# Kernel tuning notes

Hardware: AMD Instinct MI355X
Metric: run time of the kernel (lower is better)

Reference implementation:

```python
import jax, jax.numpy as jnp
import numpy as np

NUM_LAYERS = 3
DROPOUT = 0.0  # set to 0 for deterministic reference (torch F.dropout uses its own RNG)


def _spmm(rows, cols, vals, X, n_rows):
    # sparse [n_rows, n_cols] @ X[n_cols, D] via gather + segment_sum
    return jax.ops.segment_sum(vals[:, None] * X[cols], rows, num_segments=n_rows)


def setup_inputs() -> dict:
    key = jax.random.key(0)
    k1, k2, k3, k4, k5 = jax.random.split(key, 5)
    P, U, NNZ, D = 100000, 50000, 2000000, 128
    pois_embs = jax.random.normal(k1, (P, D), dtype=jnp.float32)
    up_rows = jax.random.randint(k2, (NNZ,), 0, U, dtype=jnp.int32)
    up_cols = jax.random.randint(k3, (NNZ,), 0, P, dtype=jnp.int32)
    up_vals = jax.random.uniform(k4, (NNZ,), dtype=jnp.float32)
    pu_vals = jax.random.uniform(k5, (NNZ,), dtype=jnp.float32)
    return {
        "pois_embs": pois_embs,
        "pad_all_train_sessions": jnp.zeros((1,), dtype=jnp.int64),
        "up_rows": up_rows,
        "up_cols": up_cols,
        "up_vals": up_vals,
        "pu_vals": pu_vals,
        "n_users": U,
        "n_pois": P,
    }


def reference(pois_embs, pad_all_train_sessions, up_rows, up_cols, up_vals, pu_vals, n_users, n_pois):
    # HG_up: [U, P] with entries (up_rows, up_cols, up_vals)
    # HG_pu: [P, U] = transpose structure with values pu_vals
    x = pois_embs
    acc = pois_embs  # running sum over layer outputs (incl. layer 0)
    for _ in range(NUM_LAYERS):
        msg = _spmm(up_rows, up_cols, up_vals, x, n_users)          # [U, D]
        prop = _spmm(up_cols, up_rows, pu_vals, msg, n_pois)        # [P, D]
        x = prop + x                                                 # residual
        # dropout with p=DROPOUT=0.0 -> identity
        acc = acc + x
    return acc / jnp.asarray(NUM_LAYERS + 1, dtype=pois_embs.dtype)
```

## Files before the change

kernel.cpp:

```cpp
#include <hip/hip_runtime.h>

#define DD 128
#define NUM_LAYERS 3
#define SCAN_B 1024
#define BKT_SHIFT 7
#define BKT_ROWS 128
#define LDS_BKT 1280
#define EPB 4096
#define SHARDS 4
#define CAP_SUB 1792

typedef unsigned int uint;

__device__ __forceinline__ uint f2bf(float f) {
    uint u = __float_as_uint(f);
    return (u + 0x7fffu + ((u >> 16) & 1u)) >> 16;
}
__device__ __forceinline__ uint pk2(float a, float b) {
    return f2bf(a) | (f2bf(b) << 16);
}
__device__ __forceinline__ void fma8(float acc[8], uint4 q, float v) {
    acc[0] += v * __uint_as_float(q.x << 16);
    acc[1] += v * __uint_as_float(q.x & 0xffff0000u);
    acc[2] += v * __uint_as_float(q.y << 16);
    acc[3] += v * __uint_as_float(q.y & 0xffff0000u);
    acc[4] += v * __uint_as_float(q.z << 16);
    acc[5] += v * __uint_as_float(q.z & 0xffff0000u);
    acc[6] += v * __uint_as_float(q.w << 16);
    acc[7] += v * __uint_as_float(q.w & 0xffff0000u);
}


__global__ void pass1_kernel(const int* __restrict__ up_rows,
                             const int* __restrict__ up_cols,
                             const float* __restrict__ up_vals,
                             const float* __restrict__ pu_vals,
                             int* __restrict__ bkcur,
                             int2* __restrict__ stage,
                             int nnz, int U, int nbkt) {
    __shared__ int lcnt[LDS_BKT];
    const int tid = threadIdx.x;
    const int e0 = blockIdx.x * EPB;
    const int shard = blockIdx.x & (SHARDS - 1);
    for (int i = tid; i < nbkt; i += 256) lcnt[i] = 0;
    __syncthreads();
    #pragma unroll
    for (int i = 0; i < EPB / 256; ++i) {
        const int e = e0 + i * 256 + tid;
        if (e < nnz) {
            atomicAdd(&lcnt[up_rows[e] >> BKT_SHIFT], 1);
            atomicAdd(&lcnt[(U + up_cols[e]) >> BKT_SHIFT], 1);
        }
    }
    __syncthreads();
    for (int i = tid; i < nbkt; i += 256) {
        const int c = lcnt[i];
        lcnt[i] = c ? atomicAdd(&bkcur[i * SHARDS + shard], c) : 0;
    }
    __syncthreads();
    #pragma unroll
    for (int i = 0; i < EPB / 256; ++i) {
        const int e = e0 + i * 256 + tid;
        if (e < nnz) {
            const int u = up_rows[e];
            const int p = up_cols[e];
            const int pc = U + p;
            int b = u >> BKT_SHIFT;
            int pos = atomicAdd(&lcnt[b], 1);
            if (pos < CAP_SUB)
                stage[((size_t)b * SHARDS + shard) * CAP_SUB + pos] =
                    make_int2(((u & (BKT_ROWS - 1)) << 25) | p, __float_as_int(up_vals[e]));
            b = pc >> BKT_SHIFT;
            pos = atomicAdd(&lcnt[b], 1);
            if (pos < CAP_SUB)
                stage[((size_t)b * SHARDS + shard) * CAP_SUB + pos] =
                    make_int2(((pc & (BKT_ROWS - 1)) << 25) | u, __float_as_int(pu_vals[e]));
        }
    }
}


__global__ void tot_kernel(const int* __restrict__ bkcur, int* __restrict__ tot, int nbkt) {
    const int b = blockIdx.x * blockDim.x + threadIdx.x;
    if (b >= nbkt) return;
    int t = 0;
    #pragma unroll
    for (int s = 0; s < SHARDS; ++s) t += min(bkcur[b * SHARDS + s], CAP_SUB);
    tot[b] = t;
}

__global__ void scan_blocks_kernel(const int* __restrict__ in, int* __restrict__ out,
                                   int* __restrict__ bsums, int n) {
    __shared__ int tmp[SCAN_B];
    const int tid = threadIdx.x;
    const int gid = blockIdx.x * SCAN_B + tid;
    const int v = (gid < n) ? in[gid] : 0;
    tmp[tid] = v;
    __syncthreads();
    for (int ofs = 1; ofs < SCAN_B; ofs <<= 1) {
        int t = (tid >= ofs) ? tmp[tid - ofs] : 0;
        __syncthreads();
        tmp[tid] += t;
        __syncthreads();
    }
    if (gid < n) out[gid] = tmp[tid] - v;
    if (tid == SCAN_B - 1) bsums[blockIdx.x] = tmp[tid];
}

__global__ void scan_sums_kernel(int* __restrict__ bsums, int nb) {
    __shared__ int tmp[SCAN_B];
    const int tid = threadIdx.x;
    const int v = (tid < nb) ? bsums[tid] : 0;
    tmp[tid] = v;
    __syncthreads();
    for (int ofs = 1; ofs < SCAN_B; ofs <<= 1) {
        int t = (tid >= ofs) ? tmp[tid - ofs] : 0;
        __syncthreads();
        tmp[tid] += t;
        __syncthreads();
    }
    if (tid < nb) bsums[tid] = tmp[tid] - v;
}

__global__ void scan_add_kernel(int* __restrict__ off, const int* __restrict__ bsums,
                                const int* __restrict__ cnt, int n) {
    const int gid = blockIdx.x * SCAN_B + threadIdx.x;
    if (gid >= n) return;
    const int v = off[gid] + bsums[blockIdx.x];
    off[gid] = v;
    if (gid == n - 1) off[n] = v + cnt[gid];
}


__global__ void pass2_kernel(const int* __restrict__ bkcur,
                             const int2* __restrict__ stage,
                             const int* __restrict__ bkbase,
                             int* __restrict__ off,
                             int2* __restrict__ adj, int N, int nbkt) {
    __shared__ int ca[BKT_ROWS], cb[BKT_ROWS], lcur[BKT_ROWS];
    const int b = blockIdx.x;
    const int tid = threadIdx.x;
    if (tid < BKT_ROWS) ca[tid] = 0;
    __syncthreads();
    int ns[SHARDS];
    const int2* bs[SHARDS];
    #pragma unroll
    for (int s = 0; s < SHARDS; ++s) {
        ns[s] = min(bkcur[b * SHARDS + s], CAP_SUB);
        bs[s] = stage + ((size_t)b * SHARDS + s) * CAP_SUB;
    }
    #pragma unroll
    for (int s = 0; s < SHARDS; ++s)
        for (int i = tid; i < ns[s]; i += 256)
            atomicAdd(&ca[((uint)bs[s][i].x) >> 25], 1);
    __syncthreads();
    int* src = ca; int* dst = cb;
    for (int ofs = 1; ofs < BKT_ROWS; ofs <<= 1) {
        if (tid < BKT_ROWS)
            dst[tid] = src[tid] + (tid >= ofs ? src[tid - ofs] : 0);
        __syncthreads();
        int* t = src; src = dst; dst = t;
    }
    const int base = bkbase[b];
    if (tid < BKT_ROWS) {
        const int excl = base + (tid ? src[tid - 1] : 0);
        lcur[tid] = excl;
        const int r = b * BKT_ROWS + tid;
        if (r < N) off[r] = excl;
    }
    if (b == 0 && tid == 0) off[N] = bkbase[nbkt];
    __syncthreads();
    #pragma unroll
    for (int s = 0; s < SHARDS; ++s)
        for (int i = tid; i < ns[s]; i += 256) {
            const int2 ev = bs[s][i];
            const int pos = atomicAdd(&lcur[((uint)ev.x) >> 25], 1);
            adj[pos] = make_int2(ev.x & 0x1ffffff, ev.y);
        }
}

__global__ void cvt_kernel(const float4* __restrict__ src, uint2* __restrict__ dst, int n4) {
    const int i = blockIdx.x * blockDim.x + threadIdx.x;
    if (i >= n4) return;
    const float4 f = src[i];
    dst[i] = make_uint2(pk2(f.x, f.y), pk2(f.z, f.w));
}


__global__ void spmm_u_kernel(const int* __restrict__ off,
                              const int2* __restrict__ adj,
                              const uint4* __restrict__ xbf,
                              uint4* __restrict__ msgbf, int U) {
    const int g = threadIdx.x >> 4;
    const int lane = threadIdx.x & 15;
    const int row = blockIdx.x * 16 + g;
    if (row >= U) return;
    int k = off[row];
    const int end = off[row + 1];
    float acc[8] = {0, 0, 0, 0, 0, 0, 0, 0};
    for (; k + 3 < end; k += 4) {
        const int2 e0 = adj[k];
        const int2 e1 = adj[k + 1];
        const int2 e2 = adj[k + 2];
        const int2 e3 = adj[k + 3];
        const uint4 q0 = xbf[(size_t)e0.x * 16 + lane];
        const uint4 q1 = xbf[(size_t)e1.x * 16 + lane];
        const uint4 q2 = xbf[(size_t)e2.x * 16 + lane];
        const uint4 q3 = xbf[(size_t)e3.x * 16 + lane];
        fma8(acc, q0, __int_as_float(e0.y));
        fma8(acc, q1, __int_as_float(e1.y));
        fma8(acc, q2, __int_as_float(e2.y));
        fma8(acc, q3, __int_as_float(e3.y));
    }
    for (; k < end; ++k) {
        const int2 e = adj[k];
        const uint4 q = xbf[(size_t)e.x * 16 + lane];
        fma8(acc, q, __int_as_float(e.y));
    }
    uint4 o;
    o.x = pk2(acc[0], acc[1]);
    o.y = pk2(acc[2], acc[3]);
    o.z = pk2(acc[4], acc[5]);
    o.w = pk2(acc[6], acc[7]);
    msgbf[(size_t)row * 16 + lane] = o;
}

__global__ void spmm_p_fused_kernel(const int* __restrict__ off,
                                    const int2* __restrict__ adj,
                                    const uint4* __restrict__ msgbf,
                                    uint4* __restrict__ xbf,
                                    const float4* __restrict__ embs,
                                    float4* __restrict__ out,
                                    float w, int first, int last, int U, int P) {
    const int g = threadIdx.x >> 4;
    const int lane = threadIdx.x & 15;
    const int row = blockIdx.x * 16 + g;
    if (row >= P) return;
    int k = off[U + row];
    const int end = off[U + row + 1];
    float acc[8] = {0, 0, 0, 0, 0, 0, 0, 0};
    for (; k + 3 < end; k += 4) {
        const int2 e0 = adj[k];
        const int2 e1 = adj[k + 1];
        const int2 e2 = adj[k + 2];
        const int2 e3 = adj[k + 3];
        const uint4 q0 = msgbf[(size_t)e0.x * 16 + lane];
        const uint4 q1 = msgbf[(size_t)e1.x * 16 + lane];
        const uint4 q2 = msgbf[(size_t)e2.x * 16 + lane];
        const uint4 q3 = msgbf[(size_t)e3.x * 16 + lane];
        fma8(acc, q0, __int_as_float(e0.y));
        fma8(acc, q1, __int_as_float(e1.y));
        fma8(acc, q2, __int_as_float(e2.y));
        fma8(acc, q3, __int_as_float(e3.y));
    }
    for (; k < end; ++k) {
        const int2 e = adj[k];
        const uint4 q = msgbf[(size_t)e.x * 16 + lane];
        fma8(acc, q, __int_as_float(e.y));
    }
    const size_t xi = (size_t)row * 16 + lane;
    if (!last) {
        const uint4 xq = xbf[xi];
        uint4 xn;
        xn.x = pk2(__uint_as_float(xq.x << 16) + acc[0],
                   __uint_as_float(xq.x & 0xffff0000u) + acc[1]);
        xn.y = pk2(__uint_as_float(xq.y << 16) + acc[2],
                   __uint_as_float(xq.y & 0xffff0000u) + acc[3]);
        xn.z = pk2(__uint_as_float(xq.z << 16) + acc[4],
                   __uint_as_float(xq.z & 0xffff0000u) + acc[5]);
        xn.w = pk2(__uint_as_float(xq.w << 16) + acc[6],
                   __uint_as_float(xq.w & 0xffff0000u) + acc[7]);
        xbf[xi] = xn;
    }
    const size_t oi = (size_t)row * 32 + lane * 2;
    const float4* base = first ? embs : (const float4*)out;
    float4 a = base[oi];
    float4 b = base[oi + 1];
    a.x += w * acc[0]; a.y += w * acc[1]; a.z += w * acc[2]; a.w += w * acc[3];
    b.x += w * acc[4]; b.y += w * acc[5]; b.z += w * acc[6]; b.w += w * acc[7];
    out[oi] = a;
    out[oi + 1] = b;
}


extern "C" void kernel_launch(void* const* d_in, const int* in_sizes, int n_in,
                              void* d_out, int out_size, void* d_ws, size_t ws_size,
                              hipStream_t stream) {
    const float* embs    = (const float*)d_in[0];
    const int*   up_rows = (const int*)d_in[2];
    const int*   up_cols = (const int*)d_in[3];
    const float* up_vals = (const float*)d_in[4];
    const float* pu_vals = (const float*)d_in[5];

    const int NNZ = in_sizes[2];
    const int P   = in_sizes[0] / DD;
    const int U   = 50000;
    const int N   = U + P;
    const int NBKT = (N + BKT_ROWS - 1) / BKT_ROWS;

    float* out = (float*)d_out;

    char* ws = (char*)d_ws;
    size_t o = 0;
    auto alloc = [&](size_t bytes) { size_t r = o; o = (o + bytes + 255) & ~255ULL; return r; };
    int*  bkcur  = (int*) (ws + alloc((size_t)NBKT * SHARDS * 4));
    int*  tot    = (int*) (ws + alloc((size_t)NBKT * 4));
    int*  bkbase = (int*) (ws + alloc((size_t)(NBKT + 1) * 4));
    int*  bsums  = (int*) (ws + alloc((size_t)SCAN_B * 4));
    int*  off    = (int*) (ws + alloc((size_t)(N + 1) * 4));
    int2* adj    = (int2*)(ws + alloc((size_t)2 * NNZ * 8));
    const size_t stage_off = alloc((size_t)NBKT * SHARDS * CAP_SUB * 8);
    int2*  stage = (int2*)(ws + stage_off);
    uint4* xbf   = (uint4*)(ws + stage_off);
    uint4* msgbf = (uint4*)(ws + stage_off + (size_t)P * DD * 2);

    hipMemsetAsync(bkcur, 0, (size_t)NBKT * SHARDS * 4, stream);
    const int p1blocks = (NNZ + EPB - 1) / EPB;
    pass1_kernel<<<p1blocks, 256, 0, stream>>>(up_rows, up_cols, up_vals, pu_vals,
                                               bkcur, stage, NNZ, U, NBKT);
    tot_kernel<<<(NBKT + 255) / 256, 256, 0, stream>>>(bkcur, tot, NBKT);
    const int NBb = (NBKT + SCAN_B - 1) / SCAN_B;
    scan_blocks_kernel<<<NBb, SCAN_B, 0, stream>>>(tot, bkbase, bsums, NBKT);
    scan_sums_kernel<<<1, SCAN_B, 0, stream>>>(bsums, NBb);
    scan_add_kernel<<<NBb, SCAN_B, 0, stream>>>(bkbase, bsums, tot, NBKT);
    pass2_kernel<<<NBKT, 256, 0, stream>>>(bkcur, stage, bkbase, off, adj, N, NBKT);

    const int n4 = P * DD / 4;
    cvt_kernel<<<(n4 + 255) / 256, 256, 0, stream>>>((const float4*)embs, (uint2*)xbf, n4);

    const int ublocks = (U + 15) / 16;
    const int pblocks = (P + 15) / 16;

    for (int layer = 0; layer < NUM_LAYERS; ++layer) {
        const float w = (float)(NUM_LAYERS - layer) / (NUM_LAYERS + 1);
        spmm_u_kernel<<<ublocks, 256, 0, stream>>>(off, adj, xbf, msgbf, U);
        spmm_p_fused_kernel<<<pblocks, 256, 0, stream>>>(
            off, adj, msgbf, xbf, (const float4*)embs, (float4*)out,
            w, layer == 0, layer == NUM_LAYERS - 1, U, P);
    }
}
```

Measured before the change: 579.5 us.

## Split feature dimension into four column slices to shrink gather working set

Each layer's two SpMMs now run four times, once per 32-column slice of the 128-wide bf16 embedding, using 4 lanes per row instead of 16. This is valid because the propagation is independent per column. Each pass gathers from a 2 MB-per-slice table that fits in cache far better than the full table, which should reduce random-gather traffic to HBM. In exchange the adjacency list is re-read four times as often, now with nontemporal loads, and the kernel launch count grows fourfold.

```diff
diff --git a/kernel.cpp b/kernel.cpp
--- a/kernel.cpp
+++ b/kernel.cpp
@@ -187,78 +187,80 @@
 }
 
 
-__global__ void spmm_u_kernel(const int* __restrict__ off,
-                              const int2* __restrict__ adj,
-                              const uint4* __restrict__ xbf,
-                              uint4* __restrict__ msgbf, int U) {
-    const int g = threadIdx.x >> 4;
-    const int lane = threadIdx.x & 15;
-    const int row = blockIdx.x * 16 + g;
+__global__ void spmm_u_q_kernel(const int* __restrict__ off,
+                                const long long* __restrict__ adj,
+                                const uint4* __restrict__ xbf,
+                                uint4* __restrict__ msgbf, int U, int q) {
+    const int g = threadIdx.x >> 2;
+    const int lane = threadIdx.x & 3;
+    const int row = blockIdx.x * 64 + g;
     if (row >= U) return;
     int k = off[row];
     const int end = off[row + 1];
+    const int qb = q * 4 + lane;
     float acc[8] = {0, 0, 0, 0, 0, 0, 0, 0};
     for (; k + 3 < end; k += 4) {
-        const int2 e0 = adj[k];
-        const int2 e1 = adj[k + 1];
-        const int2 e2 = adj[k + 2];
-        const int2 e3 = adj[k + 3];
-        const uint4 q0 = xbf[(size_t)e0.x * 16 + lane];
-        const uint4 q1 = xbf[(size_t)e1.x * 16 + lane];
-        const uint4 q2 = xbf[(size_t)e2.x * 16 + lane];
-        const uint4 q3 = xbf[(size_t)e3.x * 16 + lane];
-        fma8(acc, q0, __int_as_float(e0.y));
-        fma8(acc, q1, __int_as_float(e1.y));
-        fma8(acc, q2, __int_as_float(e2.y));
-        fma8(acc, q3, __int_as_float(e3.y));
+        const long long a0 = __builtin_nontemporal_load(adj + k);
+        const long long a1 = __builtin_nontemporal_load(adj + k + 1);
+        const long long a2 = __builtin_nontemporal_load(adj + k + 2);
+        const long long a3 = __builtin_nontemporal_load(adj + k + 3);
+        const uint4 q0 = xbf[(size_t)(int)(a0 & 0xffffffffLL) * 16 + qb];
+        const uint4 q1 = xbf[(size_t)(int)(a1 & 0xffffffffLL) * 16 + qb];
+        const uint4 q2 = xbf[(size_t)(int)(a2 & 0xffffffffLL) * 16 + qb];
+        const uint4 q3 = xbf[(size_t)(int)(a3 & 0xffffffffLL) * 16 + qb];
+        fma8(acc, q0, __int_as_float((int)(a0 >> 32)));
+        fma8(acc, q1, __int_as_float((int)(a1 >> 32)));
+        fma8(acc, q2, __int_as_float((int)(a2 >> 32)));
+        fma8(acc, q3, __int_as_float((int)(a3 >> 32)));
     }
     for (; k < end; ++k) {
-        const int2 e = adj[k];
-        const uint4 q = xbf[(size_t)e.x * 16 + lane];
-        fma8(acc, q, __int_as_float(e.y));
+        const long long a = __builtin_nontemporal_load(adj + k);
+        const uint4 qq = xbf[(size_t)(int)(a & 0xffffffffLL) * 16 + qb];
+        fma8(acc, qq, __int_as_float((int)(a >> 32)));
     }
     uint4 o;
     o.x = pk2(acc[0], acc[1]);
     o.y = pk2(acc[2], acc[3]);
     o.z = pk2(acc[4], acc[5]);
     o.w = pk2(acc[6], acc[7]);
-    msgbf[(size_t)row * 16 + lane] = o;
-}
-
-__global__ void spmm_p_fused_kernel(const int* __restrict__ off,
-                                    const int2* __restrict__ adj,
-                                    const uint4* __restrict__ msgbf,
-                                    uint4* __restrict__ xbf,
-                                    const float4* __restrict__ embs,
-                                    float4* __restrict__ out,
-                                    float w, int first, int last, int U, int P) {
-    const int g = threadIdx.x >> 4;
-    const int lane = threadIdx.x & 15;
-    const int row = blockIdx.x * 16 + g;
+    msgbf[(size_t)row * 16 + qb] = o;
+}
+
+__global__ void spmm_p_q_kernel(const int* __restrict__ off,
+                                const long long* __restrict__ adj,
+                                const uint4* __restrict__ msgbf,
+                                uint4* __restrict__ xbf,
+                                const float4* __restrict__ embs,
+                                float4* __restrict__ out,
+                                float w, int first, int last, int U, int P, int q) {
+    const int g = threadIdx.x >> 2;
+    const int lane = threadIdx.x & 3;
+    const int row = blockIdx.x * 64 + g;
     if (row >= P) return;
     int k = off[U + row];
     const int end = off[U + row + 1];
+    const int qb = q * 4 + lane;
     float acc[8] = {0, 0, 0, 0, 0, 0, 0, 0};
     for (; k + 3 < end; k += 4) {
-        const int2 e0 = adj[k];
-        const int2 e1 = adj[k + 1];
-        const int2 e2 = adj[k + 2];
-        const int2 e3 = adj[k + 3];
-        const uint4 q0 = msgbf[(size_t)e0.x * 16 + lane];
-        const uint4 q1 = msgbf[(size_t)e1.x * 16 + lane];
-        const uint4 q2 = msgbf[(size_t)e2.x * 16 + lane];
-        const uint4 q3 = msgbf[(size_t)e3.x * 16 + lane];
-        fma8(acc, q0, __int_as_float(e0.y));
-        fma8(acc, q1, __int_as_float(e1.y));
-        fma8(acc, q2, __int_as_float(e2.y));
-        fma8(acc, q3, __int_as_float(e3.y));
+        const long long a0 = __builtin_nontemporal_load(adj + k);
+        const long long a1 = __builtin_nontemporal_load(adj + k + 1);
+        const long long a2 = __builtin_nontemporal_load(adj + k + 2);
+        const long long a3 = __builtin_nontemporal_load(adj + k + 3);
+        const uint4 q0 = msgbf[(size_t)(int)(a0 & 0xffffffffLL) * 16 + qb];
+        const uint4 q1 = msgbf[(size_t)(int)(a1 & 0xffffffffLL) * 16 + qb];
+        const uint4 q2 = msgbf[(size_t)(int)(a2 & 0xffffffffLL) * 16 + qb];
+        const uint4 q3 = msgbf[(size_t)(int)(a3 & 0xffffffffLL) * 16 + qb];
+        fma8(acc, q0, __int_as_float((int)(a0 >> 32)));
+        fma8(acc, q1, __int_as_float((int)(a1 >> 32)));
+        fma8(acc, q2, __int_as_float((int)(a2 >> 32)));
+        fma8(acc, q3, __int_as_float((int)(a3 >> 32)));
     }
     for (; k < end; ++k) {
-        const int2 e = adj[k];
-        const uint4 q = msgbf[(size_t)e.x * 16 + lane];
-        fma8(acc, q, __int_as_float(e.y));
-    }
-    const size_t xi = (size_t)row * 16 + lane;
+        const long long a = __builtin_nontemporal_load(adj + k);
+        const uint4 qq = msgbf[(size_t)(int)(a & 0xffffffffLL) * 16 + qb];
+        fma8(acc, qq, __int_as_float((int)(a >> 32)));
+    }
+    const size_t xi = (size_t)row * 16 + qb;
     if (!last) {
         const uint4 xq = xbf[xi];
         uint4 xn;
@@ -272,7 +274,7 @@
                    __uint_as_float(xq.w & 0xffff0000u) + acc[7]);
         xbf[xi] = xn;
     }
-    const size_t oi = (size_t)row * 32 + lane * 2;
+    const size_t oi = (size_t)row * 32 + (size_t)qb * 2;
     const float4* base = first ? embs : (const float4*)out;
     float4 a = base[oi];
     float4 b = base[oi + 1];
@@ -328,14 +330,17 @@
     const int n4 = P * DD / 4;
     cvt_kernel<<<(n4 + 255) / 256, 256, 0, stream>>>((const float4*)embs, (uint2*)xbf, n4);
 
-    const int ublocks = (U + 15) / 16;
-    const int pblocks = (P + 15) / 16;
-
-    for (int layer = 0; layer < NUM_LAYERS; ++layer) {
-        const float w = (float)(NUM_LAYERS - layer) / (NUM_LAYERS + 1);
-        spmm_u_kernel<<<ublocks, 256, 0, stream>>>(off, adj, xbf, msgbf, U);
-        spmm_p_fused_kernel<<<pblocks, 256, 0, stream>>>(
-            off, adj, msgbf, xbf, (const float4*)embs, (float4*)out,
-            w, layer == 0, layer == NUM_LAYERS - 1, U, P);
-    }
-}
+    const int ublocks = (U + 63) / 64;
+    const int pblocks = (P + 63) / 64;
+
+    for (int q = 0; q < 4; ++q) {
+        for (int layer = 0; layer < NUM_LAYERS; ++layer) {
+            const float w = (float)(NUM_LAYERS - layer) / (NUM_LAYERS + 1);
+            spmm_u_q_kernel<<<ublocks, 256, 0, stream>>>(
+                off, (const long long*)adj, xbf, msgbf, U, q);
+            spmm_p_q_kernel<<<pblocks, 256, 0, stream>>>(
+                off, (const long long*)adj, msgbf, xbf, (const float4*)embs,
+                (float4*)out, w, layer == 0, layer == NUM_LAYERS - 1, U, P, q);
+        }
+    }
+}
```

New measurement: 1.326 ms. 2.29x slower.

## Sort pass1 edges in LDS before scattering and merge bucket scan kernels

Applied to the files above, without the earlier changes.

Pass1 now counting-sorts each block's edges by bucket into shared memory, then writes them out so consecutive threads store to contiguous stage locations, replacing random per-edge global scatters. The tot and three-kernel scan chain is replaced by a single one-block kernel that sums shard counts and scans two buckets per thread. This aims to improve write coalescing in the build phase and cut launch overhead. The cost is a large LDS footprint (about 64KB+) that limits occupancy for pass1, plus extra intra-block scan work.

```diff
diff --git a/kernel.cpp b/kernel.cpp
--- a/kernel.cpp
+++ b/kernel.cpp
@@ -38,64 +38,97 @@
                              int* __restrict__ bkcur,
                              int2* __restrict__ stage,
                              int nnz, int U, int nbkt) {
-    __shared__ int lcnt[LDS_BKT];
+    __shared__ int2 ebuf[2 * EPB];
+    __shared__ unsigned short bid[2 * EPB];
+    __shared__ int cnt[LDS_BKT];
+    __shared__ int obase[LDS_BKT];
+    __shared__ int rbase[LDS_BKT];
+    __shared__ int tsum[256];
     const int tid = threadIdx.x;
     const int e0 = blockIdx.x * EPB;
+    const int ne = min(EPB, nnz - e0);
     const int shard = blockIdx.x & (SHARDS - 1);
-    for (int i = tid; i < nbkt; i += 256) lcnt[i] = 0;
-    __syncthreads();
-    #pragma unroll
-    for (int i = 0; i < EPB / 256; ++i) {
-        const int e = e0 + i * 256 + tid;
-        if (e < nnz) {
-            atomicAdd(&lcnt[up_rows[e] >> BKT_SHIFT], 1);
-            atomicAdd(&lcnt[(U + up_cols[e]) >> BKT_SHIFT], 1);
+
+    for (int i = tid; i < nbkt; i += 256) cnt[i] = 0;
+    __syncthreads();
+    for (int i = tid; i < ne; i += 256) {
+        const int e = e0 + i;
+        atomicAdd(&cnt[up_rows[e] >> BKT_SHIFT], 1);
+        atomicAdd(&cnt[(U + up_cols[e]) >> BKT_SHIFT], 1);
+    }
+    __syncthreads();
+    {
+        const int base = tid * 5;
+        int loc[5];
+        int s = 0;
+        #pragma unroll
+        for (int k = 0; k < 5; ++k) {
+            loc[k] = s;
+            const int idx = base + k;
+            s += (idx < nbkt) ? cnt[idx] : 0;
         }
+        tsum[tid] = s;
+        __syncthreads();
+        for (int ofs = 1; ofs < 256; ofs <<= 1) {
+            int t = (tid >= ofs) ? tsum[tid - ofs] : 0;
+            __syncthreads();
+            tsum[tid] += t;
+            __syncthreads();
+        }
+        const int excl = tid ? tsum[tid - 1] : 0;
+        #pragma unroll
+        for (int k = 0; k < 5; ++k) {
+            const int idx = base + k;
+            if (idx < nbkt) obase[idx] = excl + loc[k];
+        }
     }
     __syncthreads();
     for (int i = tid; i < nbkt; i += 256) {
-        const int c = lcnt[i];
-        lcnt[i] = c ? atomicAdd(&bkcur[i * SHARDS + shard], c) : 0;
-    }
-    __syncthreads();
-    #pragma unroll
-    for (int i = 0; i < EPB / 256; ++i) {
-        const int e = e0 + i * 256 + tid;
-        if (e < nnz) {
-            const int u = up_rows[e];
-            const int p = up_cols[e];
-            const int pc = U + p;
-            int b = u >> BKT_SHIFT;
-            int pos = atomicAdd(&lcnt[b], 1);
-            if (pos < CAP_SUB)
-                stage[((size_t)b * SHARDS + shard) * CAP_SUB + pos] =
-                    make_int2(((u & (BKT_ROWS - 1)) << 25) | p, __float_as_int(up_vals[e]));
-            b = pc >> BKT_SHIFT;
-            pos = atomicAdd(&lcnt[b], 1);
-            if (pos < CAP_SUB)
-                stage[((size_t)b * SHARDS + shard) * CAP_SUB + pos] =
-                    make_int2(((pc & (BKT_ROWS - 1)) << 25) | u, __float_as_int(pu_vals[e]));
-        }
-    }
-}
-
-
-__global__ void tot_kernel(const int* __restrict__ bkcur, int* __restrict__ tot, int nbkt) {
-    const int b = blockIdx.x * blockDim.x + threadIdx.x;
-    if (b >= nbkt) return;
-    int t = 0;
-    #pragma unroll
-    for (int s = 0; s < SHARDS; ++s) t += min(bkcur[b * SHARDS + s], CAP_SUB);
-    tot[b] = t;
-}
-
-__global__ void scan_blocks_kernel(const int* __restrict__ in, int* __restrict__ out,
-                                   int* __restrict__ bsums, int n) {
+        const int c = cnt[i];
+        rbase[i] = c ? atomicAdd(&bkcur[i * SHARDS + shard], c) : 0;
+        cnt[i] = obase[i];
+    }
+    __syncthreads();
+    for (int i = tid; i < ne; i += 256) {
+        const int e = e0 + i;
+        const int u = up_rows[e];
+        const int p = up_cols[e];
+        int b = u >> BKT_SHIFT;
+        int slot = atomicAdd(&cnt[b], 1);
+        ebuf[slot] = make_int2(((u & (BKT_ROWS - 1)) << 25) | p, __float_as_int(up_vals[e]));
+        bid[slot] = (unsigned short)b;
+        const int pc = U + p;
+        b = pc >> BKT_SHIFT;
+        slot = atomicAdd(&cnt[b], 1);
+        ebuf[slot] = make_int2(((pc & (BKT_ROWS - 1)) << 25) | u, __float_as_int(pu_vals[e]));
+        bid[slot] = (unsigned short)b;
+    }
+    __syncthreads();
+    const int tot = 2 * ne;
+    for (int j = tid; j < tot; j += 256) {
+        const int b = bid[j];
+        const int gp = rbase[b] + (j - obase[b]);
+        if (gp < CAP_SUB)
+            stage[((size_t)b * SHARDS + shard) * CAP_SUB + gp] = ebuf[j];
+    }
+}
+
+
+__global__ void bucket_scan_kernel(const int* __restrict__ bkcur,
+                                   int* __restrict__ bkbase, int nbkt) {
     __shared__ int tmp[SCAN_B];
     const int tid = threadIdx.x;
-    const int gid = blockIdx.x * SCAN_B + tid;
-    const int v = (gid < n) ? in[gid] : 0;
-    tmp[tid] = v;
+    const int i0 = 2 * tid, i1 = 2 * tid + 1;
+    int v0 = 0, v1 = 0;
+    if (i0 < nbkt) {
+        #pragma unroll
+        for (int s = 0; s < SHARDS; ++s) v0 += min(bkcur[i0 * SHARDS + s], CAP_SUB);
+    }
+    if (i1 < nbkt) {
+        #pragma unroll
+        for (int s = 0; s < SHARDS; ++s) v1 += min(bkcur[i1 * SHARDS + s], CAP_SUB);
+    }
+    tmp[tid] = v0 + v1;
     __syncthreads();
     for (int ofs = 1; ofs < SCAN_B; ofs <<= 1) {
         int t = (tid >= ofs) ? tmp[tid - ofs] : 0;
@@ -103,32 +136,10 @@
         tmp[tid] += t;
         __syncthreads();
     }
-    if (gid < n) out[gid] = tmp[tid] - v;
-    if (tid == SCAN_B - 1) bsums[blockIdx.x] = tmp[tid];
-}
-
-__global__ void scan_sums_kernel(int* __restrict__ bsums, int nb) {
-    __shared__ int tmp[SCAN_B];
-    const int tid = threadIdx.x;
-    const int v = (tid < nb) ? bsums[tid] : 0;
-    tmp[tid] = v;
-    __syncthreads();
-    for (int ofs = 1; ofs < SCAN_B; ofs <<= 1) {
-        int t = (tid >= ofs) ? tmp[tid - ofs] : 0;
-        __syncthreads();
-        tmp[tid] += t;
-        __syncthreads();
-    }
-    if (tid < nb) bsums[tid] = tmp[tid] - v;
-}
-
-__global__ void scan_add_kernel(int* __restrict__ off, const int* __restrict__ bsums,
-                                const int* __restrict__ cnt, int n) {
-    const int gid = blockIdx.x * SCAN_B + threadIdx.x;
-    if (gid >= n) return;
-    const int v = off[gid] + bsums[blockIdx.x];
-    off[gid] = v;
-    if (gid == n - 1) off[n] = v + cnt[gid];
+    const int excl = tid ? tmp[tid - 1] : 0;
+    if (i0 < nbkt) bkbase[i0] = excl;
+    if (i1 < nbkt) bkbase[i1] = excl + v0;
+    if (tid == SCAN_B - 1) bkbase[nbkt] = tmp[SCAN_B - 1];
 }
 
 
@@ -304,9 +315,7 @@
     size_t o = 0;
     auto alloc = [&](size_t bytes) { size_t r = o; o = (o + bytes + 255) & ~255ULL; return r; };
     int*  bkcur  = (int*) (ws + alloc((size_t)NBKT * SHARDS * 4));
-    int*  tot    = (int*) (ws + alloc((size_t)NBKT * 4));
     int*  bkbase = (int*) (ws + alloc((size_t)(NBKT + 1) * 4));
-    int*  bsums  = (int*) (ws + alloc((size_t)SCAN_B * 4));
     int*  off    = (int*) (ws + alloc((size_t)(N + 1) * 4));
     int2* adj    = (int2*)(ws + alloc((size_t)2 * NNZ * 8));
     const size_t stage_off = alloc((size_t)NBKT * SHARDS * CAP_SUB * 8);
@@ -318,11 +327,7 @@
     const int p1blocks = (NNZ + EPB - 1) / EPB;
     pass1_kernel<<<p1blocks, 256, 0, stream>>>(up_rows, up_cols, up_vals, pu_vals,
                                                bkcur, stage, NNZ, U, NBKT);
-    tot_kernel<<<(NBKT + 255) / 256, 256, 0, stream>>>(bkcur, tot, NBKT);
-    const int NBb = (NBKT + SCAN_B - 1) / SCAN_B;
-    scan_blocks_kernel<<<NBb, SCAN_B, 0, stream>>>(tot, bkbase, bsums, NBKT);
-    scan_sums_kernel<<<1, SCAN_B, 0, stream>>>(bsums, NBb);
-    scan_add_kernel<<<NBb, SCAN_B, 0, stream>>>(bkbase, bsums, tot, NBKT);
+    bucket_scan_kernel<<<1, SCAN_B, 0, stream>>>(bkcur, bkbase, NBKT);
     pass2_kernel<<<NBKT, 256, 0, stream>>>(bkcur, stage, bkbase, off, adj, N, NBKT);
 
     const int n4 = P * DD / 4;
```

After: 566.2 us. 2.3% less time.
